# Optimization experiments

Hardware: AMD Instinct MI355X
Metric: run time of the kernel (lower is better)

The kernel has to match this reference:

```python
import jax, jax.numpy as jnp
import numpy as np

BLOCK = 8
HALO = 3
HEADS = 8
DIM_HEAD = 64
DIM = 128
MAX_NEG = -3.402823466e38  # -torch.finfo(float32).max, matches the CUDA kernel


def _extract_patches(xp, nh, nw, block, K):
    # xp: [b, c, Hp, Wp] (already padded). Returns [b, c, nh, nw, K, K]
    ih = (jnp.arange(nh) * block)[:, None] + jnp.arange(K)[None, :]  # [nh, K]
    iw = (jnp.arange(nw) * block)[:, None] + jnp.arange(K)[None, :]  # [nw, K]
    return xp[..., ih[:, None, :, None], iw[None, :, None, :]]


def setup_inputs() -> dict:
    key = jax.random.key(0)
    k1, k2, k3, k4, k5 = jax.random.split(key, 5)
    inner = HEADS * DIM_HEAD
    x = jax.random.normal(k1, (4, DIM, 128, 128), dtype=jnp.float32)
    s = 1.0 / np.sqrt(DIM)
    Wq = jax.random.normal(k2, (DIM, inner), dtype=jnp.float32) * s
    Wkv = jax.random.normal(k3, (DIM, 2 * inner), dtype=jnp.float32) * s
    Wo = jax.random.normal(k4, (inner, DIM), dtype=jnp.float32) * (1.0 / np.sqrt(inner))
    bo = jax.random.normal(k5, (DIM,), dtype=jnp.float32) * 0.01
    return {"x": x, "Wq": Wq, "Wkv": Wkv, "Wo": Wo, "bo": bo}


def reference(x, Wq, Wkv, Wo, bo):
    b, c, h, w = x.shape
    block, halo, heads, dh = BLOCK, HALO, HEADS, DIM_HEAD
    K = block + 2 * halo
    nh, nw = h // block, w // block
    nb = nh * nw
    I, J = block * block, K * K
    scale = dh ** -0.5

    # queries per block: [b, nb, I, c]
    q_inp = (x.reshape(b, c, nh, block, nw, block)
              .transpose(0, 2, 4, 3, 5, 1)
              .reshape(b, nb, I, c))

    # halo key/value windows via unfold-equivalent patch extraction
    xp = jnp.pad(x, ((0, 0), (0, 0), (halo, halo), (halo, halo)))
    kv = _extract_patches(xp, nh, nw, block, K)           # [b, c, nh, nw, K, K]
    kv_inp = kv.transpose(0, 2, 3, 4, 5, 1).reshape(b, nb, J, c)

    # mask: True where the halo window overlaps padding
    ones = jnp.pad(jnp.ones((1, 1, h, w), x.dtype),
                   ((0, 0), (0, 0), (halo, halo), (halo, halo)))
    mask = (_extract_patches(ones, nh, nw, block, K).reshape(nb, J) == 0)

    q = (q_inp @ Wq).reshape(b, nb, I, heads, dh) * scale
    kvp = kv_inp @ Wkv                                    # [b, nb, J, 2*inner]
    inner = heads * dh
    k = kvp[..., :inner].reshape(b, nb, J, heads, dh)
    v = kvp[..., inner:].reshape(b, nb, J, heads, dh)

    sim = jnp.einsum('bnihd,bnjhd->bnhij', q, k)          # [b, nb, heads, I, J]
    sim = jnp.where(mask[None, :, None, None, :], MAX_NEG, sim)
    attn = jax.nn.softmax(sim, axis=-1)
    out = jnp.einsum('bnhij,bnjhd->bnihd', attn, v)       # [b, nb, I, heads, dh]

    out = out.reshape(b, nb, I, inner) @ Wo + bo          # [b, nb, I, c]
    out = (out.reshape(b, nh, nw, block, block, c)
              .transpose(0, 5, 1, 3, 2, 4)
              .reshape(b, c, h, w))
    return out
```

## Files before the change

### kernel.cpp

```cpp
#include <hip/hip_runtime.h>
#include <hip/hip_bf16.h>

typedef unsigned short u16;
typedef __attribute__((ext_vector_type(8))) short short8;
typedef __attribute__((ext_vector_type(4))) short short4v;
typedef __attribute__((ext_vector_type(4))) float float4v;

__device__ __forceinline__ u16 f2b(float f) {
    unsigned int u = __float_as_uint(f);
    return (u16)((u + 0x7fffu + ((u >> 16) & 1u)) >> 16);
}

#define MFMA(a, b, c) __builtin_amdgcn_mfma_f32_16x16x32_bf16((a), (b), (c), 0, 0, 0)

__global__ void prep_weights(const float* __restrict__ Wq,
                             const float* __restrict__ Wkv,
                             const float* __restrict__ Wo,
                             u16* __restrict__ ws)
{
    const int bid = blockIdx.x, tid = threadIdx.x;
    if (bid < 32) {
        __shared__ float wq_s[128 * 65];
        __shared__ float wk_s[32 * 65];
        const int h = bid >> 2, g = bid & 3;
        for (int i = tid; i < 8192; i += 256) {
            int c0 = i >> 6, d = i & 63;
            wq_s[c0 * 65 + d] = Wq[c0 * 512 + h * 64 + d];
        }
        for (int i = tid; i < 2048; i += 256) {
            int cl = i >> 6, d = i & 63;
            wk_s[cl * 65 + d] = Wkv[(g * 32 + cl) * 1024 + h * 64 + d];
        }
        __syncthreads();
        const int c0 = tid & 127, clb = (tid >> 7) * 16;
        float acc[16];
#pragma unroll
        for (int cc = 0; cc < 16; ++cc) acc[cc] = 0.f;
        for (int d = 0; d < 64; ++d) {
            float a = wq_s[c0 * 65 + d];
#pragma unroll
            for (int cc = 0; cc < 16; ++cc)
                acc[cc] = fmaf(a, wk_s[(clb + cc) * 65 + d], acc[cc]);
        }
#pragma unroll
        for (int cc = 0; cc < 16; ++cc)
            ws[h * 16384 + (g * 32 + clb + cc) * 128 + c0] = f2b(0.125f * acc[cc]);
    } else {
        int idx = (bid - 32) * 256 + tid;
        if (idx < 65536) {
            int h = idx >> 13, c = (idx >> 6) & 127, dv = idx & 63;
            ws[131072 + h * 8192 + dv * 128 + c] =
                f2b(Wkv[c * 1024 + 512 + h * 64 + dv]);
        } else {
            int j2 = idx - 65536;
            int cout = j2 >> 9, n = j2 & 511;
            ws[196608 + j2] = f2b(Wo[n * 128 + cout]);
        }
    }
}

__global__ __launch_bounds__(1024, 4)
void halo_attn(const float* __restrict__ xg,
               const u16* __restrict__ wqk,
               const u16* __restrict__ wvt,
               const u16* __restrict__ wot,
               const float* __restrict__ bo,
               float* __restrict__ outg)
{
    extern __shared__ u16 lds[];
    u16* s_x  = lds;
    u16* t_sw = lds + 28288;
    u16* v_sw = lds + 36992;
    u16* p_sw = lds + 51840;
    u16* o_sw = lds + 66688;
    float* s_part = (float*)((char*)lds + 142592);
    float* vmul   = (float*)((char*)lds + 143360);

    const int tid  = threadIdx.x;
    const int w    = tid >> 6;
    const int m    = tid & 15;
    const int quad = (tid & 63) >> 4;

    const int wg = (blockIdx.x >> 3) + (blockIdx.x & 7) * 128;
    const int b   = wg >> 8;
    const int blk = wg & 255;
    const int by = blk >> 4, bx = blk & 15;
    const int y0 = by * 8 - 3, x0 = bx * 8 - 3;
    const bool inb = (by >= 1) && (by <= 14) && (bx >= 1) && (bx <= 14);

    const short8 zero8 = {0, 0, 0, 0, 0, 0, 0, 0};

    for (int t = tid; t < 816; t += 1024)
        ((unsigned*)(s_x + 196 * 136))[t] = 0u;
    for (int t = tid; t < 384; t += 1024) {
        int half = t / 192, u2 = t - half * 192;
        int r = u2 / 3, ch = 26 + (u2 - r * 3);
        u16* base = half ? p_sw : v_sw;
        *(short8*)(base + r * 232 + ch * 8) = zero8;
    }
    if (tid < 224) {
        int j = tid;
        float v = 0.f;
        if (j < 196) {
            int wy = j / 14, wx = j - wy * 14;
            if (inb || (((unsigned)(y0 + wy) < 128u) && ((unsigned)(x0 + wx) < 128u)))
                v = 1.f;
        }
        vmul[j] = v;
    }
    for (int idx = tid; idx < 32768; idx += 1024) {
        int wx = idx & 15, wy = (idx >> 4) & 15, c = idx >> 8;
        if (wx < 14 && wy < 14) {
            int gy = y0 + wy, gx = x0 + wx;
            float val = 0.f;
            if (inb || (((unsigned)gy < 128u) && ((unsigned)gx < 128u)))
                val = xg[((b * 128 + c) * 128 + gy) * 128 + gx];
            s_x[(wy * 14 + wx) * 136 + c] = f2b(val);
        }
    }
    __syncthreads();

    int nt = 0, sub = 0, startjt = 0, cnt = 0;
    if (w >= 4) {
        int u = w - 4;
        nt = u & 3;
        sub = u >> 2;
        startjt = sub ? (1 + 4 * sub) : 0;
        cnt = sub ? 4 : 5;
    }

    short8 xa[4][4];
    if (w < 4) {
#pragma unroll
        for (int it = 0; it < 4; ++it) {
            int i = it * 16 + m;
            int jq = ((i >> 3) + 3) * 14 + (i & 7) + 3;
#pragma unroll
            for (int kk = 0; kk < 4; ++kk)
                xa[it][kk] = *(const short8*)(s_x + jq * 136 + kk * 32 + quad * 8);
        }
    } else {
#pragma unroll
        for (int jj = 0; jj < 4; ++jj) {
            int jt = startjt + jj;
#pragma unroll
            for (int kk = 0; kk < 4; ++kk)
                xa[jj][kk] = *(const short8*)(s_x + (jt * 16 + m) * 136 + kk * 32 + quad * 8);
        }
    }

    float4v res[2];
    res[0] = (float4v){0.f, 0.f, 0.f, 0.f};
    res[1] = (float4v){0.f, 0.f, 0.f, 0.f};

#pragma unroll 1
    for (int h = 0; h < 8; ++h) {
        if (w < 4) {
#pragma unroll
            for (int p2 = 0; p2 < 2; ++p2) {
                short8 bq[4];
#pragma unroll
                for (int kk = 0; kk < 4; ++kk)
                    bq[kk] = *(const short8*)(wqk + h * 16384 +
                                 ((2 * w + p2) * 16 + m) * 128 + kk * 32 + quad * 8);
#pragma unroll
                for (int it = 0; it < 4; ++it) {
                    float4v c = {0.f, 0.f, 0.f, 0.f};
#pragma unroll
                    for (int kk = 0; kk < 4; ++kk) c = MFMA(xa[it][kk], bq[kk], c);
#pragma unroll
                    for (int r = 0; r < 4; ++r)
                        t_sw[(it * 16 + quad * 4 + r) * 136 + (2 * w + p2) * 16 + m]
                            = f2b(c[r]);
                }
            }
        } else {
            short8 bv[4];
#pragma unroll
            for (int kk = 0; kk < 4; ++kk)
                bv[kk] = *(const short8*)(wvt + h * 8192 + (nt * 16 + m) * 128 +
                                          kk * 32 + quad * 8);
#pragma unroll
            for (int jj = 0; jj < 5; ++jj) if (jj < cnt) {
                int jt = startjt + jj;
                float4v c = {0.f, 0.f, 0.f, 0.f};
#pragma unroll
                for (int kk = 0; kk < 4; ++kk) {
                    short8 a;
                    if (jj < 4) a = xa[jj][kk];
                    else        a = *(const short8*)(s_x + (jt * 16 + m) * 136 +
                                                     kk * 32 + quad * 8);
                    c = MFMA(a, bv[kk], c);
                }
                short4v pk;
#pragma unroll
                for (int r = 0; r < 4; ++r) pk[r] = (short)f2b(c[r]);
                *(short4v*)(v_sw + (nt * 16 + m) * 232 + jt * 16 + quad * 4) = pk;
            }
        }
        __syncthreads();

        if (w >= 4) {
            const int it = nt;
            short8 ta[4];
#pragma unroll
            for (int kk = 0; kk < 4; ++kk)
                ta[kk] = *(const short8*)(t_sw + (it * 16 + m) * 136 +
                                          kk * 32 + quad * 8);
            float lsum[4] = {0.f, 0.f, 0.f, 0.f};
#pragma unroll
            for (int jj = 0; jj < 5; ++jj) if (jj < cnt) {
                int jt = startjt + jj;
                float4v c = {0.f, 0.f, 0.f, 0.f};
#pragma unroll
                for (int kk = 0; kk < 4; ++kk) {
                    short8 xb;
                    if (jj < 4) xb = xa[jj][kk];
                    else        xb = *(const short8*)(s_x + (jt * 16 + m) * 136 +
                                                      kk * 32 + quad * 8);
                    c = MFMA(ta[kk], xb, c);
                }
                int j = jt * 16 + m;
                float vm = vmul[j];
#pragma unroll
                for (int r = 0; r < 4; ++r) {
                    float p = __expf(c[r]) * vm;
                    lsum[r] += p;
                    p_sw[(it * 16 + quad * 4 + r) * 232 + j] = f2b(p);
                }
            }
#pragma unroll
            for (int mk = 1; mk < 16; mk <<= 1)
#pragma unroll
                for (int r = 0; r < 4; ++r)
                    lsum[r] += __shfl_xor(lsum[r], mk, 64);
            if (m == 0) {
#pragma unroll
                for (int r = 0; r < 4; ++r)
                    s_part[sub * 64 + it * 16 + quad * 4 + r] = lsum[r];
            }
        }
        __syncthreads();

        {
            const int it = w & 3, nt2 = w >> 2;
            float4v c = {0.f, 0.f, 0.f, 0.f};
#pragma unroll
            for (int kk = 0; kk < 7; ++kk) {
                short8 pa = *(const short8*)(p_sw + (it * 16 + m) * 232 +
                                             kk * 32 + quad * 8);
                short8 vb = *(const short8*)(v_sw + (nt2 * 16 + m) * 232 +
                                             kk * 32 + quad * 8);
                c = MFMA(pa, vb, c);
            }
#pragma unroll
            for (int r = 0; r < 4; ++r) {
                int i = it * 16 + quad * 4 + r;
                float ss = s_part[i] + s_part[64 + i] + s_part[128 + i];
                o_sw[i * 72 + nt2 * 16 + m] = f2b(c[r] / ss);
            }
        }
        __syncthreads();

        {
            const int ct = w & 7, itp = w >> 3;
            short8 bw[2];
#pragma unroll
            for (int kk = 0; kk < 2; ++kk)
                bw[kk] = *(const short8*)(wot + (ct * 16 + m) * 512 + h * 64 +
                                          kk * 32 + quad * 8);
#pragma unroll
            for (int t2 = 0; t2 < 2; ++t2) {
                int it = itp * 2 + t2;
                float4v c = res[t2];
#pragma unroll
                for (int kk = 0; kk < 2; ++kk) {
                    short8 ao = *(const short8*)(o_sw + (it * 16 + m) * 72 +
                                                 kk * 32 + quad * 8);
                    c = MFMA(ao, bw[kk], c);
                }
                res[t2] = c;
            }
        }
    }

    {
        const int ct = w & 7, itp = w >> 3;
        const int ch = ct * 16 + m;
        const float bias = bo[ch];
#pragma unroll
        for (int t2 = 0; t2 < 2; ++t2) {
#pragma unroll
            for (int r = 0; r < 4; ++r) {
                int i = (itp * 2 + t2) * 16 + quad * 4 + r;
                int gy = by * 8 + (i >> 3), gx = bx * 8 + (i & 7);
                outg[((b * 128 + ch) * 128 + gy) * 128 + gx] = res[t2][r] + bias;
            }
        }
    }
}

extern "C" void kernel_launch(void* const* d_in, const int* in_sizes, int n_in,
                              void* d_out, int out_size, void* d_ws, size_t ws_size,
                              hipStream_t stream) {
    const float* x   = (const float*)d_in[0];
    const float* Wq  = (const float*)d_in[1];
    const float* Wkv = (const float*)d_in[2];
    const float* Wo  = (const float*)d_in[3];
    const float* bo  = (const float*)d_in[4];
    float* out = (float*)d_out;
    u16* ws = (u16*)d_ws;

    prep_weights<<<dim3(544), dim3(256), 0, stream>>>(Wq, Wkv, Wo, ws);

    (void)hipFuncSetAttribute((const void*)halo_attn,
                              hipFuncAttributeMaxDynamicSharedMemorySize, 144256);
    halo_attn<<<dim3(1024), dim3(1024), 144256, stream>>>(
        x, ws, ws + 131072, ws + 196608, bo, out);
}
```

Before: 387.7 us.

## Switch attention kernel to 32x32x16 MFMA tiles with repartitioned wave work

Replaces the 16x16x32 bf16 MFMA with the 32x32x16 variant throughout the per-head pipeline and reassigns work across the 16 waves: Q projection on 8 waves, V projection on 14 tiles, scores on 14 waves, PV on 4 waves, and the output projection on 8 waves. Operands are streamed from LDS per k-chunk instead of being preloaded into registers. The softmax row sum is reduced across 32 lanes into a per-row array of 7 partials, and the LDS padding is enlarged to cover the 224-wide tiles. The aim is fewer MFMA issues and less per-tile overhead. The cost is load imbalance: some phases leave many waves idle, and LDS operand traffic goes up.

```diff
diff --git a/kernel.cpp b/kernel.cpp
--- a/kernel.cpp
+++ b/kernel.cpp
@@ -3,15 +3,23 @@
 
 typedef unsigned short u16;
 typedef __attribute__((ext_vector_type(8))) short short8;
-typedef __attribute__((ext_vector_type(4))) short short4v;
 typedef __attribute__((ext_vector_type(4))) float float4v;
+typedef __attribute__((ext_vector_type(16))) float f32x16;
+typedef __attribute__((ext_vector_type(2))) int int2v;
 
 __device__ __forceinline__ u16 f2b(float f) {
     unsigned int u = __float_as_uint(f);
     return (u16)((u + 0x7fffu + ((u >> 16) & 1u)) >> 16);
 }
 
-#define MFMA(a, b, c) __builtin_amdgcn_mfma_f32_16x16x32_bf16((a), (b), (c), 0, 0, 0)
+__device__ __forceinline__ f32x16 zero16() {
+    f32x16 z;
+#pragma unroll
+    for (int q = 0; q < 16; ++q) z[q] = 0.f;
+    return z;
+}
+
+#define MFMA32(a, b, c) __builtin_amdgcn_mfma_f32_32x32x16_bf16((a), (b), (c), 0, 0, 0)
 
 __global__ void prep_weights(const float* __restrict__ Wq,
                              const float* __restrict__ Wkv,
@@ -59,7 +67,8 @@
     }
 }
 
-__global__ __launch_bounds__(1024, 4)
+__global__
+__attribute__((amdgpu_flat_work_group_size(1024, 1024), amdgpu_waves_per_eu(4, 4)))
 void halo_attn(const float* __restrict__ xg,
                const u16* __restrict__ wqk,
                const u16* __restrict__ wvt,
@@ -69,17 +78,18 @@
 {
     extern __shared__ u16 lds[];
     u16* s_x  = lds;
-    u16* t_sw = lds + 28288;
-    u16* v_sw = lds + 36992;
-    u16* p_sw = lds + 51840;
-    u16* o_sw = lds + 66688;
-    float* s_part = (float*)((char*)lds + 142592);
-    float* vmul   = (float*)((char*)lds + 143360);
+    u16* t_sw = lds + 30464;
+    u16* v_sw = lds + 39168;
+    u16* p_sw = lds + 54016;
+    u16* o_sw = lds + 68864;
+    float* s_part = (float*)((char*)lds + 146944);
+    float* vmul   = (float*)((char*)lds + 148992);
 
     const int tid  = threadIdx.x;
     const int w    = tid >> 6;
-    const int m    = tid & 15;
-    const int quad = (tid & 63) >> 4;
+    const int lane = tid & 63;
+    const int n5   = lane & 31;
+    const int half = lane >> 5;
 
     const int wg = (blockIdx.x >> 3) + (blockIdx.x & 7) * 128;
     const int b   = wg >> 8;
@@ -88,16 +98,9 @@
     const int y0 = by * 8 - 3, x0 = bx * 8 - 3;
     const bool inb = (by >= 1) && (by <= 14) && (bx >= 1) && (bx <= 14);
 
-    const short8 zero8 = {0, 0, 0, 0, 0, 0, 0, 0};
-
-    for (int t = tid; t < 816; t += 1024)
+    for (int t = tid; t < 1904; t += 1024)
         ((unsigned*)(s_x + 196 * 136))[t] = 0u;
-    for (int t = tid; t < 384; t += 1024) {
-        int half = t / 192, u2 = t - half * 192;
-        int r = u2 / 3, ch = 26 + (u2 - r * 3);
-        u16* base = half ? p_sw : v_sw;
-        *(short8*)(base + r * 232 + ch * 8) = zero8;
-    }
+    if (tid < 512) ((unsigned*)s_part)[tid] = 0u;
     if (tid < 224) {
         int j = tid;
         float v = 0.f;
@@ -120,182 +123,137 @@
     }
     __syncthreads();
 
-    int nt = 0, sub = 0, startjt = 0, cnt = 0;
-    if (w >= 4) {
-        int u = w - 4;
-        nt = u & 3;
-        sub = u >> 2;
-        startjt = sub ? (1 + 4 * sub) : 0;
-        cnt = sub ? 4 : 5;
-    }
-
-    short8 xa[4][4];
-    if (w < 4) {
-#pragma unroll
-        for (int it = 0; it < 4; ++it) {
-            int i = it * 16 + m;
-            int jq = ((i >> 3) + 3) * 14 + (i & 7) + 3;
-#pragma unroll
-            for (int kk = 0; kk < 4; ++kk)
-                xa[it][kk] = *(const short8*)(s_x + jq * 136 + kk * 32 + quad * 8);
-        }
-    } else {
-#pragma unroll
-        for (int jj = 0; jj < 4; ++jj) {
-            int jt = startjt + jj;
-#pragma unroll
-            for (int kk = 0; kk < 4; ++kk)
-                xa[jj][kk] = *(const short8*)(s_x + (jt * 16 + m) * 136 + kk * 32 + quad * 8);
-        }
-    }
-
-    float4v res[2];
-    res[0] = (float4v){0.f, 0.f, 0.f, 0.f};
-    res[1] = (float4v){0.f, 0.f, 0.f, 0.f};
+    f32x16 res = zero16();
 
 #pragma unroll 1
     for (int h = 0; h < 8; ++h) {
+        if (w < 8) {
+            const int c4 = w >> 1;
+            const int i = (w & 1) * 32 + n5;
+            const int jq = ((i >> 3) + 3) * 14 + (i & 7) + 3;
+            f32x16 acc = zero16();
+#pragma unroll
+            for (int kc = 0; kc < 8; ++kc) {
+                short8 a  = *(const short8*)(s_x + jq * 136 + kc * 16 + half * 8);
+                short8 bq = *(const short8*)(wqk + h * 16384 +
+                                             (c4 * 32 + n5) * 128 + kc * 16 + half * 8);
+                acc = MFMA32(a, bq, acc);
+            }
+#pragma unroll
+            for (int q = 0; q < 16; ++q) {
+                int rq = (q & 3) + 8 * (q >> 2) + 4 * half;
+                t_sw[((w & 1) * 32 + rq) * 136 + c4 * 32 + n5] = f2b(acc[q]);
+            }
+        }
+        {
+            const int vt = (w >= 8) ? (w - 8) : (w < 6 ? 8 + w : -1);
+            if (vt >= 0) {
+                const int j7 = vt % 7, dv2 = vt / 7;
+                f32x16 acc = zero16();
+#pragma unroll
+                for (int kc = 0; kc < 8; ++kc) {
+                    short8 a  = *(const short8*)(s_x + (j7 * 32 + n5) * 136 +
+                                                 kc * 16 + half * 8);
+                    short8 bv = *(const short8*)(wvt + h * 8192 +
+                                                 (dv2 * 32 + n5) * 128 + kc * 16 + half * 8);
+                    acc = MFMA32(a, bv, acc);
+                }
+#pragma unroll
+                for (int g = 0; g < 4; ++g) {
+                    unsigned lo = (unsigned)f2b(acc[4 * g + 0]) |
+                                  ((unsigned)f2b(acc[4 * g + 1]) << 16);
+                    unsigned hi = (unsigned)f2b(acc[4 * g + 2]) |
+                                  ((unsigned)f2b(acc[4 * g + 3]) << 16);
+                    int2v pk; pk[0] = (int)lo; pk[1] = (int)hi;
+                    *(int2v*)(v_sw + (dv2 * 32 + n5) * 232 +
+                              j7 * 32 + 8 * g + 4 * half) = pk;
+                }
+            }
+        }
+        __syncthreads();
+
+        if (w < 14) {
+            const int si = w & 1, j7 = w >> 1;
+            f32x16 acc = zero16();
+#pragma unroll
+            for (int kc = 0; kc < 8; ++kc) {
+                short8 ta = *(const short8*)(t_sw + (si * 32 + n5) * 136 +
+                                             kc * 16 + half * 8);
+                short8 xb = *(const short8*)(s_x + (j7 * 32 + n5) * 136 +
+                                             kc * 16 + half * 8);
+                acc = MFMA32(ta, xb, acc);
+            }
+            const int j = j7 * 32 + n5;
+            const float vm = vmul[j];
+#pragma unroll
+            for (int q = 0; q < 16; ++q) {
+                int rq = (q & 3) + 8 * (q >> 2) + 4 * half;
+                float p = __expf(acc[q]) * vm;
+                p_sw[(si * 32 + rq) * 232 + j] = f2b(p);
+                acc[q] = p;
+            }
+#pragma unroll
+            for (int mk = 1; mk < 32; mk <<= 1)
+#pragma unroll
+                for (int q = 0; q < 16; ++q)
+                    acc[q] += __shfl_xor(acc[q], mk, 64);
+            if (n5 == 0) {
+#pragma unroll
+                for (int q = 0; q < 16; ++q) {
+                    int rq = (q & 3) + 8 * (q >> 2) + 4 * half;
+                    s_part[(si * 32 + rq) * 8 + j7] = acc[q];
+                }
+            }
+        }
+        __syncthreads();
+
         if (w < 4) {
-#pragma unroll
-            for (int p2 = 0; p2 < 2; ++p2) {
-                short8 bq[4];
-#pragma unroll
-                for (int kk = 0; kk < 4; ++kk)
-                    bq[kk] = *(const short8*)(wqk + h * 16384 +
-                                 ((2 * w + p2) * 16 + m) * 128 + kk * 32 + quad * 8);
-#pragma unroll
-                for (int it = 0; it < 4; ++it) {
-                    float4v c = {0.f, 0.f, 0.f, 0.f};
-#pragma unroll
-                    for (int kk = 0; kk < 4; ++kk) c = MFMA(xa[it][kk], bq[kk], c);
-#pragma unroll
-                    for (int r = 0; r < 4; ++r)
-                        t_sw[(it * 16 + quad * 4 + r) * 136 + (2 * w + p2) * 16 + m]
-                            = f2b(c[r]);
-                }
-            }
-        } else {
-            short8 bv[4];
-#pragma unroll
-            for (int kk = 0; kk < 4; ++kk)
-                bv[kk] = *(const short8*)(wvt + h * 8192 + (nt * 16 + m) * 128 +
-                                          kk * 32 + quad * 8);
-#pragma unroll
-            for (int jj = 0; jj < 5; ++jj) if (jj < cnt) {
-                int jt = startjt + jj;
-                float4v c = {0.f, 0.f, 0.f, 0.f};
-#pragma unroll
-                for (int kk = 0; kk < 4; ++kk) {
-                    short8 a;
-                    if (jj < 4) a = xa[jj][kk];
-                    else        a = *(const short8*)(s_x + (jt * 16 + m) * 136 +
-                                                     kk * 32 + quad * 8);
-                    c = MFMA(a, bv[kk], c);
-                }
-                short4v pk;
-#pragma unroll
-                for (int r = 0; r < 4; ++r) pk[r] = (short)f2b(c[r]);
-                *(short4v*)(v_sw + (nt * 16 + m) * 232 + jt * 16 + quad * 4) = pk;
-            }
-        }
-        __syncthreads();
-
-        if (w >= 4) {
-            const int it = nt;
-            short8 ta[4];
-#pragma unroll
-            for (int kk = 0; kk < 4; ++kk)
-                ta[kk] = *(const short8*)(t_sw + (it * 16 + m) * 136 +
-                                          kk * 32 + quad * 8);
-            float lsum[4] = {0.f, 0.f, 0.f, 0.f};
-#pragma unroll
-            for (int jj = 0; jj < 5; ++jj) if (jj < cnt) {
-                int jt = startjt + jj;
-                float4v c = {0.f, 0.f, 0.f, 0.f};
-#pragma unroll
-                for (int kk = 0; kk < 4; ++kk) {
-                    short8 xb;
-                    if (jj < 4) xb = xa[jj][kk];
-                    else        xb = *(const short8*)(s_x + (jt * 16 + m) * 136 +
-                                                      kk * 32 + quad * 8);
-                    c = MFMA(ta[kk], xb, c);
-                }
-                int j = jt * 16 + m;
-                float vm = vmul[j];
-#pragma unroll
-                for (int r = 0; r < 4; ++r) {
-                    float p = __expf(c[r]) * vm;
-                    lsum[r] += p;
-                    p_sw[(it * 16 + quad * 4 + r) * 232 + j] = f2b(p);
-                }
-            }
-#pragma unroll
-            for (int mk = 1; mk < 16; mk <<= 1)
-#pragma unroll
-                for (int r = 0; r < 4; ++r)
-                    lsum[r] += __shfl_xor(lsum[r], mk, 64);
-            if (m == 0) {
-#pragma unroll
-                for (int r = 0; r < 4; ++r)
-                    s_part[sub * 64 + it * 16 + quad * 4 + r] = lsum[r];
-            }
-        }
-        __syncthreads();
-
-        {
-            const int it = w & 3, nt2 = w >> 2;
-            float4v c = {0.f, 0.f, 0.f, 0.f};
-#pragma unroll
-            for (int kk = 0; kk < 7; ++kk) {
-                short8 pa = *(const short8*)(p_sw + (it * 16 + m) * 232 +
-                                             kk * 32 + quad * 8);
-                short8 vb = *(const short8*)(v_sw + (nt2 * 16 + m) * 232 +
-                                             kk * 32 + quad * 8);
-                c = MFMA(pa, vb, c);
-            }
-#pragma unroll
-            for (int r = 0; r < 4; ++r) {
-                int i = it * 16 + quad * 4 + r;
-                float ss = s_part[i] + s_part[64 + i] + s_part[128 + i];
-                o_sw[i * 72 + nt2 * 16 + m] = f2b(c[r] / ss);
-            }
-        }
-        __syncthreads();
-
-        {
-            const int ct = w & 7, itp = w >> 3;
-            short8 bw[2];
-#pragma unroll
-            for (int kk = 0; kk < 2; ++kk)
-                bw[kk] = *(const short8*)(wot + (ct * 16 + m) * 512 + h * 64 +
-                                          kk * 32 + quad * 8);
-#pragma unroll
-            for (int t2 = 0; t2 < 2; ++t2) {
-                int it = itp * 2 + t2;
-                float4v c = res[t2];
-#pragma unroll
-                for (int kk = 0; kk < 2; ++kk) {
-                    short8 ao = *(const short8*)(o_sw + (it * 16 + m) * 72 +
-                                                 kk * 32 + quad * 8);
-                    c = MFMA(ao, bw[kk], c);
-                }
-                res[t2] = c;
-            }
-        }
-    }
-
-    {
-        const int ct = w & 7, itp = w >> 3;
-        const int ch = ct * 16 + m;
+            const int pi = w & 1, dv2 = w >> 1;
+            f32x16 acc = zero16();
+#pragma unroll
+            for (int kc = 0; kc < 14; ++kc) {
+                short8 pa = *(const short8*)(p_sw + (pi * 32 + n5) * 232 +
+                                             kc * 16 + half * 8);
+                short8 vb = *(const short8*)(v_sw + (dv2 * 32 + n5) * 232 +
+                                             kc * 16 + half * 8);
+                acc = MFMA32(pa, vb, acc);
+            }
+#pragma unroll
+            for (int q = 0; q < 16; ++q) {
+                int rq = (q & 3) + 8 * (q >> 2) + 4 * half;
+                int row = pi * 32 + rq;
+                float4v s0 = *(const float4v*)(s_part + row * 8);
+                float4v s1 = *(const float4v*)(s_part + row * 8 + 4);
+                float ss = ((s0[0] + s0[1]) + (s0[2] + s0[3])) +
+                           ((s1[0] + s1[1]) + s1[2]);
+                o_sw[row * 72 + dv2 * 32 + n5] = f2b(acc[q] / ss);
+            }
+        }
+        __syncthreads();
+
+        if (w < 8) {
+            const int c4 = w >> 1, ei = w & 1;
+#pragma unroll
+            for (int kc = 0; kc < 4; ++kc) {
+                short8 ao = *(const short8*)(o_sw + (ei * 32 + n5) * 72 +
+                                             kc * 16 + half * 8);
+                short8 bw = *(const short8*)(wot + (c4 * 32 + n5) * 512 + h * 64 +
+                                             kc * 16 + half * 8);
+                res = MFMA32(ao, bw, res);
+            }
+        }
+    }
+
+    if (w < 8) {
+        const int c4 = w >> 1, ei = w & 1;
+        const int ch = c4 * 32 + n5;
         const float bias = bo[ch];
 #pragma unroll
-        for (int t2 = 0; t2 < 2; ++t2) {
-#pragma unroll
-            for (int r = 0; r < 4; ++r) {
-                int i = (itp * 2 + t2) * 16 + quad * 4 + r;
-                int gy = by * 8 + (i >> 3), gx = bx * 8 + (i & 7);
-                outg[((b * 128 + ch) * 128 + gy) * 128 + gx] = res[t2][r] + bias;
-            }
+        for (int q = 0; q < 16; ++q) {
+            int rq = (q & 3) + 8 * (q >> 2) + 4 * half;
+            int i = ei * 32 + rq;
+            int gy = by * 8 + (i >> 3), gx = bx * 8 + (i & 7);
+            outg[((b * 128 + ch) * 128 + gy) * 128 + gx] = res[q] + bias;
         }
     }
 }
@@ -314,7 +272,7 @@
     prep_weights<<<dim3(544), dim3(256), 0, stream>>>(Wq, Wkv, Wo, ws);
 
     (void)hipFuncSetAttribute((const void*)halo_attn,
-                              hipFuncAttributeMaxDynamicSharedMemorySize, 144256);
-    halo_attn<<<dim3(1024), dim3(1024), 144256, stream>>>(
+                              hipFuncAttributeMaxDynamicSharedMemorySize, 149888);
+    halo_attn<<<dim3(1024), dim3(1024), 149888, stream>>>(
         x, ws, ws + 131072, ws + 196608, bo, out);
 }
```

Result: slower. 521.0 us (+34.4%).
